# Optimization experiments

Measured on AMD Instinct MI355X. Metric: run time of the kernel, lower is better.

The kernel has to match this reference:

```python
import jax, jax.numpy as jnp
from jax import lax
import numpy as np
import itertools

R = 7            # resolution
N = R * R        # 49 tokens
H = 8            # num_heads
KD = 32          # key_dim
QKD = 2 * H * KD # 512
VD = 2 * KD * H  # 512 (attn_ratio * key_dim * num_heads)
DIM = 384
B = 2048
SCALE = KD ** (-0.5)
BN_EPS = 1e-5


def _bias_idxs():
    points = list(itertools.product(range(R), range(R)))
    offsets = {}
    idxs = []
    for p1 in points:
        for p2 in points:
            o = (abs(p1[0] - p2[0]), abs(p1[1] - p2[1]))
            if o not in offsets:
                offsets[o] = len(offsets)
            idxs.append(offsets[o])
    return np.asarray(idxs, dtype=np.int32).reshape(N, N)  # [49,49], values in [0,49)


def setup_inputs() -> dict:
    key = jax.random.key(0)
    ks = jax.random.split(key, 8)
    return {
        "x": jax.random.normal(ks[0], (B, N, DIM), jnp.float32),
        "pwconv_w": jax.random.normal(ks[1], (QKD + VD, DIM), jnp.float32) * 0.05,
        "pwconv_b": jax.random.normal(ks[2], (QKD + VD,), jnp.float32) * 0.05,
        "dw_w": jax.random.normal(ks[3], (VD, 1, 3, 3), jnp.float32) * 0.1,
        "bn_gamma": jnp.ones((VD,), jnp.float32),
        "bn_beta": jnp.zeros((VD,), jnp.float32),
        "bn_mean": jnp.zeros((VD,), jnp.float32),
        "bn_var": jnp.ones((VD,), jnp.float32),
        "attn_biases": jax.random.normal(ks[4], (H, 49), jnp.float32) * 0.02,
        "proj_w": jax.random.normal(ks[5], (DIM, VD), jnp.float32) * 0.05,
        "proj_b": jnp.zeros((DIM,), jnp.float32),
        "bias_idxs": jnp.asarray(_bias_idxs()),
    }


def reference(x, pwconv_w, pwconv_b, dw_w, bn_gamma, bn_beta, bn_mean, bn_var,
              attn_biases, proj_w, proj_b, bias_idxs):
    b = x.shape[0]
    # [B,N,C] -> [B,C,7,7]
    xc = x.transpose(0, 2, 1).reshape(b, DIM, R, R)
    # 1x1 conv (pointwise) as einsum
    h = jnp.einsum('bchw,oc->bohw', xc, pwconv_w) + pwconv_b[None, :, None, None]
    qk, v1 = h[:, :QKD], h[:, QKD:]
    # [B,512,7,7] -> [B,2,H,KD,N] -> [2,B,H,N,KD]
    qk = qk.reshape(b, 2, H, KD, N).transpose(1, 0, 2, 4, 3)
    q, k = qk[0], qk[1]
    # depthwise 3x3 conv + BN (inference form) + exact GELU, residual into v1
    dw = lax.conv_general_dilated(v1, dw_w, (1, 1), 'SAME',
                                  feature_group_count=VD,
                                  dimension_numbers=('NCHW', 'OIHW', 'NCHW'))
    dw = (dw - bn_mean[None, :, None, None]) * (bn_gamma[None, :, None, None]
          * lax.rsqrt(bn_var[None, :, None, None] + BN_EPS)) + bn_beta[None, :, None, None]
    v1 = v1 + jax.nn.gelu(dw, approximate=False)
    # [B,VD,7,7] -> [B,H,dv,N] -> [B,H,N,dv]
    v = v1.reshape(b, H, VD // H, N).transpose(0, 1, 3, 2)
    bias = attn_biases[:, bias_idxs]  # [H,N,N] gathered relative-position bias
    attn = jax.nn.softmax(jnp.einsum('bhnd,bhmd->bhnm', q, k) * SCALE + bias[None], axis=-1)
    out = jnp.einsum('bhnm,bhmd->bhnd', attn, v).transpose(0, 2, 1, 3).reshape(b, N, VD)
    return out @ proj_w.T + proj_b
```

## Files before the change

kernel.cpp:

```cpp
#include <hip/hip_runtime.h>
#include <hip/hip_bf16.h>

#define NPOS 49
#define NH 8
#define DIMC 384
#define VDC 512
#define SCALE_QK 0.17677669529663687f

typedef unsigned short u16;
typedef __attribute__((ext_vector_type(8))) short bf16x8_t;
typedef __attribute__((ext_vector_type(4))) float f32x4_t;

__device__ __forceinline__ u16 f2bf(float f) {
    unsigned u = __float_as_uint(f);
    u = (u + 0x7fffu + ((u >> 16) & 1u)) >> 16;
    return (u16)u;
}
__device__ __forceinline__ float bf2f(u16 b) {
    return __uint_as_float(((unsigned)b) << 16);
}

__global__ __launch_bounds__(256) void prep_kernel(
    const float* __restrict__ pw, const float* __restrict__ pj,
    const float* __restrict__ ab, const int* __restrict__ bidx,
    u16* __restrict__ wpw, u16* __restrict__ wpj, float* __restrict__ biasf)
{
    int i = blockIdx.x * 256 + threadIdx.x;
    if (i < 1024 * 384) wpw[i] = f2bf(pw[i]);
    if (i < 384 * 512)  wpj[i] = f2bf(pj[i]);
    if (i < 8 * 49 * 49) {
        int h = i / (49 * 49);
        int nm = i - h * (49 * 49);
        biasf[i] = ab[h * 49 + bidx[nm]];
    }
}

__global__ __launch_bounds__(512) void fused_kernel(
    const float* __restrict__ x,
    const float* __restrict__ pwb,
    const float* __restrict__ dww,
    const float* __restrict__ bng, const float* __restrict__ bnb,
    const float* __restrict__ bnm, const float* __restrict__ bnv,
    const float* __restrict__ pjb,
    const u16* __restrict__ wpw, const u16* __restrict__ wpj,
    const float* __restrict__ biasf,
    float* __restrict__ out)
{
    __shared__ u16 lds[68224];
    const int tid  = threadIdx.x;
    const int b    = blockIdx.x;
    const int wv   = tid >> 6;
    const int lane = tid & 63;
    const int quad = lane >> 4;
    const int l16  = lane & 15;

    u16* s_x  = lds;
    u16* s_q  = lds;
    u16* s_k  = lds + 15680;
    u16* s_P  = lds;
    u16* s_v  = lds + 31360;
    u16* s_o2 = lds + 31360;

    const float* xb = x + (size_t)b * (NPOS * DIMC);
    for (int i = tid; i < NPOS * DIMC; i += 512) {
        int n = i / DIMC;
        int c = i - n * DIMC;
        s_x[n * 392 + c] = f2bf(xb[i]);
    }
    for (int i = tid; i < 512 * 23; i += 512) {
        int c = i / 23, j = i - c * 23;
        s_v[c * 72 + 49 + j] = 0;
    }
    __syncthreads();

    f32x4_t acc[8][4];
    #pragma unroll
    for (int nt = 0; nt < 8; ++nt)
        #pragma unroll
        for (int mt = 0; mt < 4; ++mt)
            acc[nt][mt] = (f32x4_t){0.f, 0.f, 0.f, 0.f};

    #pragma unroll
    for (int ks = 0; ks < 12; ++ks) {
        const int k0 = ks * 32 + quad * 8;
        bf16x8_t afr[4];
        #pragma unroll
        for (int mt = 0; mt < 4; ++mt)
            afr[mt] = *(const bf16x8_t*)(s_x + (mt * 16 + l16) * 392 + k0);
        #pragma unroll
        for (int nt = 0; nt < 8; ++nt) {
            const int och = wv * 128 + nt * 16 + l16;
            bf16x8_t bfr = *(const bf16x8_t*)(wpw + och * 384 + k0);
            #pragma unroll
            for (int mt = 0; mt < 4; ++mt)
                acc[nt][mt] = __builtin_amdgcn_mfma_f32_16x16x32_bf16(
                    afr[mt], bfr, acc[nt][mt], 0, 0, 0);
        }
    }
    __syncthreads();

    #pragma unroll
    for (int nt = 0; nt < 8; ++nt) {
        const int och = wv * 128 + nt * 16 + l16;
        const float bias = pwb[och];
        u16* dst;
        int stride;
        if (och < 256)      { dst = s_q + ((och >> 5) * 49) * 40 + (och & 31); stride = 40; }
        else if (och < 512) { int o2 = och - 256;
                              dst = s_k + ((o2 >> 5) * 49) * 40 + (o2 & 31); stride = 40; }
        else                { dst = s_v + (och - 512) * 72; stride = 1; }
        #pragma unroll
        for (int mt = 0; mt < 4; ++mt)
            #pragma unroll
            for (int r = 0; r < 4; ++r) {
                int pos = mt * 16 + quad * 4 + r;
                if (pos < 49) dst[pos * stride] = f2bf(acc[nt][mt][r] + bias);
            }
    }
    __syncthreads();

    {
        const int c = tid;
        u16* src = s_v + c * 72;
        float vv[49];
        #pragma unroll
        for (int i = 0; i < 49; ++i) vv[i] = bf2f(src[i]);
        float tap[9];
        #pragma unroll
        for (int j = 0; j < 9; ++j) tap[j] = dww[c * 9 + j];
        const float scale = bng[c] * rsqrtf(bnv[c] + 1e-5f);
        const float shift = bnb[c] - bnm[c] * scale;
        float res[49];
        #pragma unroll
        for (int y = 0; y < 7; ++y)
            #pragma unroll
            for (int xx = 0; xx < 7; ++xx) {
                float s = 0.f;
                #pragma unroll
                for (int ky = 0; ky < 3; ++ky)
                    #pragma unroll
                    for (int kx = 0; kx < 3; ++kx) {
                        int iy = y + ky - 1, ix = xx + kx - 1;
                        if (iy >= 0 && iy < 7 && ix >= 0 && ix < 7)
                            s += tap[ky * 3 + kx] * vv[iy * 7 + ix];
                    }
                s = s * scale + shift;
                float g = 0.5f * s * (1.0f + erff(s * 0.70710678118654752f));
                res[y * 7 + xx] = vv[y * 7 + xx] + g;
            }
        #pragma unroll
        for (int i = 0; i < 49; ++i) src[i] = f2bf(res[i]);
    }
    __syncthreads();

    {
        const int h = wv;
        bf16x8_t qa[4], kfr[4];
        #pragma unroll
        for (int mt = 0; mt < 4; ++mt)
            qa[mt] = *(const bf16x8_t*)(s_q + (h * 49 + mt * 16 + l16) * 40 + quad * 8);
        #pragma unroll
        for (int nt = 0; nt < 4; ++nt)
            kfr[nt] = *(const bf16x8_t*)(s_k + (h * 49 + nt * 16 + l16) * 40 + quad * 8);
        f32x4_t sc[4][4];
        #pragma unroll
        for (int mt = 0; mt < 4; ++mt)
            #pragma unroll
            for (int nt = 0; nt < 4; ++nt) {
                f32x4_t z = (f32x4_t){0.f, 0.f, 0.f, 0.f};
                sc[mt][nt] = __builtin_amdgcn_mfma_f32_16x16x32_bf16(qa[mt], kfr[nt], z, 0, 0, 0);
            }

        float pvreg[4][4][4];
        #pragma unroll
        for (int mt = 0; mt < 4; ++mt)
            #pragma unroll
            for (int r = 0; r < 4; ++r) {
                const int qrow = mt * 16 + quad * 4 + r;
                float sv[4];
                #pragma unroll
                for (int nt = 0; nt < 4; ++nt) {
                    const int key = nt * 16 + l16;
                    float val = sc[mt][nt][r] * SCALE_QK;
                    if (key < 49 && qrow < 49) val += biasf[(h * 49 + qrow) * 49 + key];
                    else                       val = -1e30f;
                    sv[nt] = val;
                }
                float mx = fmaxf(fmaxf(sv[0], sv[1]), fmaxf(sv[2], sv[3]));
                #pragma unroll
                for (int off = 1; off < 16; off <<= 1)
                    mx = fmaxf(mx, __shfl_xor(mx, off));
                float e0 = __expf(sv[0] - mx), e1 = __expf(sv[1] - mx);
                float e2 = __expf(sv[2] - mx), e3 = __expf(sv[3] - mx);
                float sum = e0 + e1 + e2 + e3;
                #pragma unroll
                for (int off = 1; off < 16; off <<= 1)
                    sum += __shfl_xor(sum, off);
                const float inv = 1.0f / sum;
                pvreg[mt][r][0] = e0 * inv; pvreg[mt][r][1] = e1 * inv;
                pvreg[mt][r][2] = e2 * inv; pvreg[mt][r][3] = e3 * inv;
            }
        __syncthreads();
        #pragma unroll
        for (int mt = 0; mt < 4; ++mt)
            #pragma unroll
            for (int r = 0; r < 4; ++r) {
                const int qrow = mt * 16 + quad * 4 + r;
                if (qrow < 49) {
                    #pragma unroll
                    for (int nt = 0; nt < 4; ++nt)
                        s_P[(h * 49 + qrow) * 72 + nt * 16 + l16] = f2bf(pvreg[mt][r][nt]);
                }
            }
        __syncthreads();

        f32x4_t oa[4][4];
        #pragma unroll
        for (int mt = 0; mt < 4; ++mt)
            #pragma unroll
            for (int nt = 0; nt < 4; ++nt)
                oa[mt][nt] = (f32x4_t){0.f, 0.f, 0.f, 0.f};
        #pragma unroll
        for (int ksv = 0; ksv < 2; ++ksv) {
            const int kb0 = ksv * 32 + quad * 8;
            bf16x8_t pa[4], vb[4];
            #pragma unroll
            for (int mt = 0; mt < 4; ++mt)
                pa[mt] = *(const bf16x8_t*)(s_P + (h * 49 + mt * 16 + l16) * 72 + kb0);
            #pragma unroll
            for (int nt = 0; nt < 4; ++nt)
                vb[nt] = *(const bf16x8_t*)(s_v + (h * 64 + nt * 16 + l16) * 72 + kb0);
            #pragma unroll
            for (int mt = 0; mt < 4; ++mt)
                #pragma unroll
                for (int nt = 0; nt < 4; ++nt)
                    oa[mt][nt] = __builtin_amdgcn_mfma_f32_16x16x32_bf16(
                        pa[mt], vb[nt], oa[mt][nt], 0, 0, 0);
        }
        __syncthreads();
        #pragma unroll
        for (int mt = 0; mt < 4; ++mt)
            #pragma unroll
            for (int nt = 0; nt < 4; ++nt)
                #pragma unroll
                for (int r = 0; r < 4; ++r) {
                    int pos = mt * 16 + quad * 4 + r;
                    if (pos < 49)
                        s_o2[pos * 520 + h * 64 + nt * 16 + l16] = f2bf(oa[mt][nt][r]);
                }
    }
    __syncthreads();

    {
        f32x4_t pacc[3][4];
        #pragma unroll
        for (int ntl = 0; ntl < 3; ++ntl)
            #pragma unroll
            for (int mt = 0; mt < 4; ++mt)
                pacc[ntl][mt] = (f32x4_t){0.f, 0.f, 0.f, 0.f};
        #pragma unroll
        for (int ks = 0; ks < 16; ++ks) {
            const int k0 = ks * 32 + quad * 8;
            bf16x8_t afr[4];
            #pragma unroll
            for (int mt = 0; mt < 4; ++mt)
                afr[mt] = *(const bf16x8_t*)(s_o2 + (mt * 16 + l16) * 520 + k0);
            #pragma unroll
            for (int ntl = 0; ntl < 3; ++ntl) {
                const int o = (wv * 3 + ntl) * 16 + l16;
                bf16x8_t wb = *(const bf16x8_t*)(wpj + o * 512 + k0);
                #pragma unroll
                for (int mt = 0; mt < 4; ++mt)
                    pacc[ntl][mt] = __builtin_amdgcn_mfma_f32_16x16x32_bf16(
                        afr[mt], wb, pacc[ntl][mt], 0, 0, 0);
            }
        }
        float* ob = out + (size_t)b * (NPOS * DIMC);
        #pragma unroll
        for (int ntl = 0; ntl < 3; ++ntl) {
            const int o = (wv * 3 + ntl) * 16 + l16;
            const float pb = pjb[o];
            #pragma unroll
            for (int mt = 0; mt < 4; ++mt)
                #pragma unroll
                for (int r = 0; r < 4; ++r) {
                    int pos = mt * 16 + quad * 4 + r;
                    if (pos < 49) ob[pos * 384 + o] = pacc[ntl][mt][r] + pb;
                }
        }
    }
}

extern "C" void kernel_launch(void* const* d_in, const int* in_sizes, int n_in,
                              void* d_out, int out_size, void* d_ws, size_t ws_size,
                              hipStream_t stream)
{
    const float* x   = (const float*)d_in[0];
    const float* pw  = (const float*)d_in[1];
    const float* pwb = (const float*)d_in[2];
    const float* dww = (const float*)d_in[3];
    const float* bng = (const float*)d_in[4];
    const float* bnb = (const float*)d_in[5];
    const float* bnm = (const float*)d_in[6];
    const float* bnv = (const float*)d_in[7];
    const float* ab  = (const float*)d_in[8];
    const float* pj  = (const float*)d_in[9];
    const float* pjb = (const float*)d_in[10];
    const int*  bidx = (const int*)d_in[11];
    float* out = (float*)d_out;

    u16* wpw   = (u16*)d_ws;
    u16* wpj   = wpw + 1024 * 384;
    float* bia = (float*)(wpj + 384 * 512);

    const int nb = in_sizes[0] / (NPOS * DIMC);

    prep_kernel<<<1536, 256, 0, stream>>>(pw, pj, ab, bidx, wpw, wpj, bia);
    fused_kernel<<<nb, 512, 0, stream>>>(x, pwb, dww, bng, bnb, bnm, bnv, pjb,
                                         wpw, wpj, bia, out);
}
```

Before: 717.6 us.

## Tile-swizzle weights and LDS buffers, stage bf16 bias in LDS, vectorize loads

The prep kernel now reorders the pointwise and projection weights into 16x32 MFMA tiles, so each lane fragment load reads contiguous memory. It also stores the relative-position bias as bf16, and each block copies that bias into LDS instead of reading it from global memory during softmax. The q/k, v and P buffers in LDS use XOR-swizzled layouts with power-of-two row strides to avoid bank conflicts, and x loads and the v stores/loads are vectorized. Softmax normalization is deferred to the PV output, and launch bounds request 2 blocks per CU. The extra LDS and register pressure may limit occupancy, and the bias is rounded to bf16.

```diff
diff --git a/kernel.cpp b/kernel.cpp
--- a/kernel.cpp
+++ b/kernel.cpp
@@ -1,5 +1,4 @@
 #include <hip/hip_runtime.h>
-#include <hip/hip_bf16.h>
 
 #define NPOS 49
 #define NH 8
@@ -8,6 +7,7 @@
 #define SCALE_QK 0.17677669529663687f
 
 typedef unsigned short u16;
+typedef unsigned int u32;
 typedef __attribute__((ext_vector_type(8))) short bf16x8_t;
 typedef __attribute__((ext_vector_type(4))) float f32x4_t;
 
@@ -23,19 +23,25 @@
 __global__ __launch_bounds__(256) void prep_kernel(
     const float* __restrict__ pw, const float* __restrict__ pj,
     const float* __restrict__ ab, const int* __restrict__ bidx,
-    u16* __restrict__ wpw, u16* __restrict__ wpj, float* __restrict__ biasf)
+    u16* __restrict__ wpw, u16* __restrict__ wpj, u16* __restrict__ biasb)
 {
     int i = blockIdx.x * 256 + threadIdx.x;
-    if (i < 1024 * 384) wpw[i] = f2bf(pw[i]);
-    if (i < 384 * 512)  wpj[i] = f2bf(pj[i]);
+    if (i < 1024 * 384) {
+        int och = i / 384, k = i - och * 384;
+        wpw[((och >> 4) * 12 + (k >> 5)) * 512 + (och & 15) * 32 + (k & 31)] = f2bf(pw[i]);
+    }
+    if (i < 384 * 512) {
+        int o = i / 512, k = i - o * 512;
+        wpj[((o >> 4) * 16 + (k >> 5)) * 512 + (o & 15) * 32 + (k & 31)] = f2bf(pj[i]);
+    }
     if (i < 8 * 49 * 49) {
         int h = i / (49 * 49);
         int nm = i - h * (49 * 49);
-        biasf[i] = ab[h * 49 + bidx[nm]];
-    }
-}
-
-__global__ __launch_bounds__(512) void fused_kernel(
+        biasb[i] = f2bf(ab[h * 49 + bidx[nm]]);
+    }
+}
+
+__global__ __launch_bounds__(512, 2) void fused_kernel(
     const float* __restrict__ x,
     const float* __restrict__ pwb,
     const float* __restrict__ dww,
@@ -43,10 +49,10 @@
     const float* __restrict__ bnm, const float* __restrict__ bnv,
     const float* __restrict__ pjb,
     const u16* __restrict__ wpw, const u16* __restrict__ wpj,
-    const float* __restrict__ biasf,
+    const u16* __restrict__ biasb,
     float* __restrict__ out)
 {
-    __shared__ u16 lds[68224];
+    __shared__ u16 lds[77064];
     const int tid  = threadIdx.x;
     const int b    = blockIdx.x;
     const int wv   = tid >> 6;
@@ -56,20 +62,24 @@
 
     u16* s_x  = lds;
     u16* s_q  = lds;
-    u16* s_k  = lds + 15680;
+    u16* s_k  = lds + 12544;
     u16* s_P  = lds;
-    u16* s_v  = lds + 31360;
-    u16* s_o2 = lds + 31360;
-
-    const float* xb = x + (size_t)b * (NPOS * DIMC);
-    for (int i = tid; i < NPOS * DIMC; i += 512) {
-        int n = i / DIMC;
-        int c = i - n * DIMC;
-        s_x[n * 392 + c] = f2bf(xb[i]);
-    }
-    for (int i = tid; i < 512 * 23; i += 512) {
-        int c = i / 23, j = i - c * 23;
-        s_v[c * 72 + 49 + j] = 0;
+    u16* s_v  = lds + 25088;
+    u16* s_o2 = lds + 25088;
+    u16* s_bs = lds + 57856;
+
+    {
+        const float4* xb4 = (const float4*)(x + (size_t)b * (NPOS * DIMC));
+        for (int f = tid; f < NPOS * 96; f += 512) {
+            float4 v = xb4[f];
+            int row = f / 96;
+            int cc  = (f - row * 96) * 4;
+            ushort4 w;
+            w.x = f2bf(v.x); w.y = f2bf(v.y); w.z = f2bf(v.z); w.w = f2bf(v.w);
+            *(ushort4*)(s_x + row * 392 + cc) = w;
+        }
+        for (int i = tid; i < 9604; i += 512)
+            ((u32*)s_bs)[i] = ((const u32*)biasb)[i];
     }
     __syncthreads();
 
@@ -89,8 +99,8 @@
             afr[mt] = *(const bf16x8_t*)(s_x + (mt * 16 + l16) * 392 + k0);
         #pragma unroll
         for (int nt = 0; nt < 8; ++nt) {
-            const int och = wv * 128 + nt * 16 + l16;
-            bf16x8_t bfr = *(const bf16x8_t*)(wpw + och * 384 + k0);
+            bf16x8_t bfr = *(const bf16x8_t*)(
+                wpw + ((wv * 8 + nt) * 12 + ks) * 512 + l16 * 32 + quad * 8);
             #pragma unroll
             for (int mt = 0; mt < 4; ++mt)
                 acc[nt][mt] = __builtin_amdgcn_mfma_f32_16x16x32_bf16(
@@ -103,34 +113,60 @@
     for (int nt = 0; nt < 8; ++nt) {
         const int och = wv * 128 + nt * 16 + l16;
         const float bias = pwb[och];
-        u16* dst;
-        int stride;
-        if (och < 256)      { dst = s_q + ((och >> 5) * 49) * 40 + (och & 31); stride = 40; }
-        else if (och < 512) { int o2 = och - 256;
-                              dst = s_k + ((o2 >> 5) * 49) * 40 + (o2 & 31); stride = 40; }
-        else                { dst = s_v + (och - 512) * 72; stride = 1; }
-        #pragma unroll
-        for (int mt = 0; mt < 4; ++mt)
-            #pragma unroll
-            for (int r = 0; r < 4; ++r) {
-                int pos = mt * 16 + quad * 4 + r;
-                if (pos < 49) dst[pos * stride] = f2bf(acc[nt][mt][r] + bias);
-            }
+        if (och < 512) {
+            const int isk = och >> 8;
+            const int hh  = (och >> 5) & 7;
+            const int d   = och & 31;
+            u16* base = isk ? s_k : s_q;
+            #pragma unroll
+            for (int mt = 0; mt < 4; ++mt)
+                #pragma unroll
+                for (int r = 0; r < 4; ++r) {
+                    int pos = mt * 16 + quad * 4 + r;
+                    if (pos < 49) {
+                        int rowi = hh * 49 + pos;
+                        int dblk = (d >> 3) ^ ((rowi >> 2) & 3);
+                        base[rowi * 32 + (dblk << 3) + (d & 7)] =
+                            f2bf(acc[nt][mt][r] + bias);
+                    }
+                }
+        } else {
+            const int c  = och - 512;
+            const int cb = c & 7;
+            u16* vrow = s_v + c * 64;
+            #pragma unroll
+            for (int mt = 0; mt < 4; ++mt) {
+                int pos0 = mt * 16 + quad * 4;
+                int jb   = pos0 >> 3;
+                int off  = pos0 & 7;
+                ushort4 w;
+                w.x = f2bf(acc[nt][mt][0] + bias);
+                w.y = f2bf(acc[nt][mt][1] + bias);
+                w.z = f2bf(acc[nt][mt][2] + bias);
+                w.w = f2bf(acc[nt][mt][3] + bias);
+                *(ushort4*)(vrow + ((jb ^ cb) << 3) + off) = w;
+            }
+        }
     }
     __syncthreads();
 
     {
-        const int c = tid;
-        u16* src = s_v + c * 72;
-        float vv[49];
-        #pragma unroll
-        for (int i = 0; i < 49; ++i) vv[i] = bf2f(src[i]);
+        const int c  = tid;
+        const int cb = c & 7;
+        u16* vrow = s_v + c * 64;
+        float vv[56];
+        #pragma unroll
+        for (int jb = 0; jb < 7; ++jb) {
+            bf16x8_t t = *(const bf16x8_t*)(vrow + ((jb ^ cb) << 3));
+            #pragma unroll
+            for (int e = 0; e < 8; ++e) vv[jb * 8 + e] = bf2f((u16)t[e]);
+        }
         float tap[9];
         #pragma unroll
         for (int j = 0; j < 9; ++j) tap[j] = dww[c * 9 + j];
         const float scale = bng[c] * rsqrtf(bnv[c] + 1e-5f);
         const float shift = bnb[c] - bnm[c] * scale;
-        float res[49];
+        float res[64];
         #pragma unroll
         for (int y = 0; y < 7; ++y)
             #pragma unroll
@@ -149,19 +185,33 @@
                 res[y * 7 + xx] = vv[y * 7 + xx] + g;
             }
         #pragma unroll
-        for (int i = 0; i < 49; ++i) src[i] = f2bf(res[i]);
-    }
-    __syncthreads();
-
+        for (int i = 49; i < 64; ++i) res[i] = 0.f;
+        #pragma unroll
+        for (int jb = 0; jb < 8; ++jb) {
+            bf16x8_t t;
+            #pragma unroll
+            for (int e = 0; e < 8; ++e) t[e] = (short)f2bf(res[jb * 8 + e]);
+            *(bf16x8_t*)(vrow + ((jb ^ cb) << 3)) = t;
+        }
+    }
+    __syncthreads();
+
+    float invr[4][4];
     {
         const int h = wv;
         bf16x8_t qa[4], kfr[4];
         #pragma unroll
-        for (int mt = 0; mt < 4; ++mt)
-            qa[mt] = *(const bf16x8_t*)(s_q + (h * 49 + mt * 16 + l16) * 40 + quad * 8);
-        #pragma unroll
-        for (int nt = 0; nt < 4; ++nt)
-            kfr[nt] = *(const bf16x8_t*)(s_k + (h * 49 + nt * 16 + l16) * 40 + quad * 8);
+        for (int mt = 0; mt < 4; ++mt) {
+            int row = h * 49 + mt * 16 + l16;
+            int jq  = quad ^ ((row >> 2) & 3);
+            qa[mt] = *(const bf16x8_t*)(s_q + row * 32 + (jq << 3));
+        }
+        #pragma unroll
+        for (int nt = 0; nt < 4; ++nt) {
+            int row = h * 49 + nt * 16 + l16;
+            int jq  = quad ^ ((row >> 2) & 3);
+            kfr[nt] = *(const bf16x8_t*)(s_k + row * 32 + (jq << 3));
+        }
         f32x4_t sc[4][4];
         #pragma unroll
         for (int mt = 0; mt < 4; ++mt)
@@ -182,8 +232,10 @@
                 for (int nt = 0; nt < 4; ++nt) {
                     const int key = nt * 16 + l16;
                     float val = sc[mt][nt][r] * SCALE_QK;
-                    if (key < 49 && qrow < 49) val += biasf[(h * 49 + qrow) * 49 + key];
-                    else                       val = -1e30f;
+                    if (key < 49 && qrow < 49)
+                        val += bf2f(s_bs[(h * 49 + qrow) * 49 + key]);
+                    else
+                        val = -1e30f;
                     sv[nt] = val;
                 }
                 float mx = fmaxf(fmaxf(sv[0], sv[1]), fmaxf(sv[2], sv[3]));
@@ -196,9 +248,9 @@
                 #pragma unroll
                 for (int off = 1; off < 16; off <<= 1)
                     sum += __shfl_xor(sum, off);
-                const float inv = 1.0f / sum;
-                pvreg[mt][r][0] = e0 * inv; pvreg[mt][r][1] = e1 * inv;
-                pvreg[mt][r][2] = e2 * inv; pvreg[mt][r][3] = e3 * inv;
+                invr[mt][r] = 1.0f / sum;
+                pvreg[mt][r][0] = e0; pvreg[mt][r][1] = e1;
+                pvreg[mt][r][2] = e2; pvreg[mt][r][3] = e3;
             }
         __syncthreads();
         #pragma unroll
@@ -207,9 +259,12 @@
             for (int r = 0; r < 4; ++r) {
                 const int qrow = mt * 16 + quad * 4 + r;
                 if (qrow < 49) {
+                    const int rp = h * 49 + qrow;
+                    const int rb = rp & 7;
                     #pragma unroll
                     for (int nt = 0; nt < 4; ++nt)
-                        s_P[(h * 49 + qrow) * 72 + nt * 16 + l16] = f2bf(pvreg[mt][r][nt]);
+                        s_P[rp * 64 + (((2 * nt + (l16 >> 3)) ^ rb) << 3) + (l16 & 7)] =
+                            f2bf(pvreg[mt][r][nt]);
                 }
             }
         __syncthreads();
@@ -222,14 +277,18 @@
                 oa[mt][nt] = (f32x4_t){0.f, 0.f, 0.f, 0.f};
         #pragma unroll
         for (int ksv = 0; ksv < 2; ++ksv) {
-            const int kb0 = ksv * 32 + quad * 8;
+            const int jblk = ksv * 4 + quad;
             bf16x8_t pa[4], vb[4];
             #pragma unroll
-            for (int mt = 0; mt < 4; ++mt)
-                pa[mt] = *(const bf16x8_t*)(s_P + (h * 49 + mt * 16 + l16) * 72 + kb0);
-            #pragma unroll
-            for (int nt = 0; nt < 4; ++nt)
-                vb[nt] = *(const bf16x8_t*)(s_v + (h * 64 + nt * 16 + l16) * 72 + kb0);
+            for (int mt = 0; mt < 4; ++mt) {
+                int rp = h * 49 + mt * 16 + l16;
+                pa[mt] = *(const bf16x8_t*)(s_P + rp * 64 + ((jblk ^ (rp & 7)) << 3));
+            }
+            #pragma unroll
+            for (int nt = 0; nt < 4; ++nt) {
+                int rv = h * 64 + nt * 16 + l16;
+                vb[nt] = *(const bf16x8_t*)(s_v + rv * 64 + ((jblk ^ (rv & 7)) << 3));
+            }
             #pragma unroll
             for (int mt = 0; mt < 4; ++mt)
                 #pragma unroll
@@ -246,7 +305,8 @@
                 for (int r = 0; r < 4; ++r) {
                     int pos = mt * 16 + quad * 4 + r;
                     if (pos < 49)
-                        s_o2[pos * 520 + h * 64 + nt * 16 + l16] = f2bf(oa[mt][nt][r]);
+                        s_o2[pos * 520 + h * 64 + nt * 16 + l16] =
+                            f2bf(oa[mt][nt][r] * invr[mt][r]);
                 }
     }
     __syncthreads();
@@ -267,8 +327,8 @@
                 afr[mt] = *(const bf16x8_t*)(s_o2 + (mt * 16 + l16) * 520 + k0);
             #pragma unroll
             for (int ntl = 0; ntl < 3; ++ntl) {
-                const int o = (wv * 3 + ntl) * 16 + l16;
-                bf16x8_t wb = *(const bf16x8_t*)(wpj + o * 512 + k0);
+                bf16x8_t wb = *(const bf16x8_t*)(
+                    wpj + ((wv * 3 + ntl) * 16 + ks) * 512 + l16 * 32 + quad * 8);
                 #pragma unroll
                 for (int mt = 0; mt < 4; ++mt)
                     pacc[ntl][mt] = __builtin_amdgcn_mfma_f32_16x16x32_bf16(
@@ -311,11 +371,11 @@
 
     u16* wpw   = (u16*)d_ws;
     u16* wpj   = wpw + 1024 * 384;
-    float* bia = (float*)(wpj + 384 * 512);
+    u16* biasb = wpj + 384 * 512;
 
     const int nb = in_sizes[0] / (NPOS * DIMC);
 
-    prep_kernel<<<1536, 256, 0, stream>>>(pw, pj, ab, bidx, wpw, wpj, bia);
+    prep_kernel<<<1536, 256, 0, stream>>>(pw, pj, ab, bidx, wpw, wpj, biasb);
     fused_kernel<<<nb, 512, 0, stream>>>(x, pwb, dww, bng, bnb, bnm, bnv, pjb,
-                                         wpw, wpj, bia, out);
-}
+                                         wpw, wpj, biasb, out);
+}
```

Result: faster. 684.6 us (-4.6%).
